# Performance work log

Hardware: AMD Instinct MI355X
Metric: run time of the kernel (lower is better)

## Reference

```python
import jax, jax.numpy as jnp
import numpy as np

# DeepSpeed FixedSparsityConfig defaults (attention='unidirectional')
BLOCK = 16
NUM_LOCAL_BLOCKS = 4   # local window = 4 blocks = 64 tokens
D_MODEL = 1024
N_HEADS = 16
HEAD_DIM = D_MODEL // N_HEADS


def _block_layout(seq_len: int) -> np.ndarray:
    """Token-level boolean mask [S,S] from the fixed unidirectional block layout.
    Allowed iff: (same 4-block local window AND block_k <= block_q) OR
                 (block_k % 4 == 3 AND block_k <= block_q)  (causal global column).
    Same layout for every head (different_layout_per_head=False)."""
    nb = seq_len // BLOCK
    r = np.arange(nb)
    causal = r[None, :] <= r[:, None]
    same_win = (r[:, None] // NUM_LOCAL_BLOCKS) == (r[None, :] // NUM_LOCAL_BLOCKS)
    glob = (r[None, :] % NUM_LOCAL_BLOCKS) == (NUM_LOCAL_BLOCKS - 1)
    layout = (same_win & causal) | (glob & causal)
    return np.kron(layout, np.ones((BLOCK, BLOCK), dtype=bool))


def setup_inputs() -> dict:
    key = jax.random.key(0)
    ks = jax.random.split(key, 7)
    B, S = 2, 2048
    init = 1.0 / np.sqrt(D_MODEL)
    x = jax.random.normal(ks[0], (B, S, D_MODEL), jnp.float32)
    key_padding_mask = jnp.zeros((B, S), jnp.float32)  # additive mask ('add' mode)
    Wq = jax.random.normal(ks[1], (D_MODEL, D_MODEL), jnp.float32) * init
    Wk = jax.random.normal(ks[2], (D_MODEL, D_MODEL), jnp.float32) * init
    Wv = jax.random.normal(ks[3], (D_MODEL, D_MODEL), jnp.float32) * init
    bq = jax.random.normal(ks[4], (D_MODEL,), jnp.float32) * 0.01
    bk = jax.random.normal(ks[5], (D_MODEL,), jnp.float32) * 0.01
    bv = jax.random.normal(ks[6], (D_MODEL,), jnp.float32) * 0.01
    return dict(x=x, key_padding_mask=key_padding_mask,
                Wq=Wq, bq=bq, Wk=Wk, bk=bk, Wv=Wv, bv=bv)


def reference(x, key_padding_mask, Wq, bq, Wk, bk, Wv, bv):
    B, S, D = x.shape
    q = (x @ Wq + bq).reshape(B, S, N_HEADS, HEAD_DIM)
    k = (x @ Wk + bk).reshape(B, S, N_HEADS, HEAD_DIM)
    v = (x @ Wv + bv).reshape(B, S, N_HEADS, HEAD_DIM)
    scale = HEAD_DIM ** -0.5  # DeepSpeed scales by head_size**-0.5 inside softmax
    scores = jnp.einsum('bqhd,bkhd->bhqk', q, k) * scale
    scores = scores + key_padding_mask[:, None, None, :]
    mask = jnp.asarray(_block_layout(S))  # [S,S] bool; absent blocks excluded from softmax
    scores = jnp.where(mask[None, None], scores, -jnp.inf)
    attn = jax.nn.softmax(scores, axis=-1)
    out = jnp.einsum('bhqk,bkhd->bqhd', attn, v)
    return out.reshape(B, S, D)
```

## Files before the change

### kernel.cpp

```cpp
#include <hip/hip_runtime.h>
#include <hip/hip_bf16.h>

typedef __bf16 bf16;
typedef __bf16 bf16x4 __attribute__((ext_vector_type(4)));
typedef __bf16 bf16x8 __attribute__((ext_vector_type(8)));
typedef float  f32x4  __attribute__((ext_vector_type(4)));

#define D_MODEL 1024
#define S_LEN   2048
#define BATCH   2
#define NH      16
#define HD      64
#define NX ((size_t)BATCH * S_LEN * D_MODEL)

__device__ inline void gl_lds16(const bf16* g, bf16* l) {
    __builtin_amdgcn_global_load_lds(
        (const __attribute__((address_space(1))) void*)g,
        (__attribute__((address_space(3))) void*)l, 16, 0, 0);
}

__global__ __launch_bounds__(256) void cvt_x(
    const float* __restrict__ x, bf16* __restrict__ xb)
{
    const size_t base = ((size_t)blockIdx.x * 256 + threadIdx.x) * 8;
    const float4 a = *(const float4*)(x + base);
    const float4 b = *(const float4*)(x + base + 4);
    bf16x8 o;
    o[0] = (bf16)a.x; o[1] = (bf16)a.y; o[2] = (bf16)a.z; o[3] = (bf16)a.w;
    o[4] = (bf16)b.x; o[5] = (bf16)b.y; o[6] = (bf16)b.z; o[7] = (bf16)b.w;
    *(bf16x8*)(xb + base) = o;
}

__global__ __launch_bounds__(256) void wt_cvt(
    const float* __restrict__ Wq, const float* __restrict__ Wk,
    const float* __restrict__ Wv, bf16* __restrict__ Wt)
{
    const int z = blockIdx.z;
    const float* W = (z == 0) ? Wq : (z == 1) ? Wk : Wv;
    const int k0 = blockIdx.y * 64, n0 = blockIdx.x * 64;

    __shared__ bf16 tile[64 * 72];

    const int r16 = threadIdx.x >> 4, c4 = (threadIdx.x & 15) << 2;

#pragma unroll
    for (int rr = 0; rr < 4; ++rr) {
        const int row = rr * 16 + r16;
        const float4 v = *(const float4*)(W + (size_t)(k0 + row) * D_MODEL + n0 + c4);
        bf16x4 o; o[0] = (bf16)v.x; o[1] = (bf16)v.y; o[2] = (bf16)v.z; o[3] = (bf16)v.w;
        *(bf16x4*)(tile + row * 72 + c4) = o;
    }
    __syncthreads();
#pragma unroll
    for (int rr = 0; rr < 4; ++rr) {
        const int row = rr * 16 + r16;
        bf16x4 o;
#pragma unroll
        for (int j = 0; j < 4; ++j) o[j] = tile[(c4 + j) * 72 + row];
        *(bf16x4*)(Wt + (size_t)(z * D_MODEL + n0 + row) * D_MODEL + k0 + c4) = o;
    }
}

__global__ __launch_bounds__(256) void gemm_bt(
    const bf16* __restrict__ Xb, const bf16* __restrict__ Wt,
    const float* __restrict__ bq, const float* __restrict__ bk,
    const float* __restrict__ bv, bf16* __restrict__ QKV)
{
    const int n0 = blockIdx.x * 128, m0 = blockIdx.y * 128;
    const int z  = n0 >> 10;
    const float* bias = (z == 0) ? bq : (z == 1) ? bk : bv;
    const float scale = (z == 0) ? 0.125f : 1.0f;
    bf16* C = QKV + (size_t)z * NX;
    const int ncol0 = n0 & 1023;

    __shared__ bf16 As[128 * 32];
    __shared__ bf16 Bs[128 * 32];

    const int t = threadIdx.x, wave = t >> 6, lane = t & 63;
    const int wm = wave >> 1, wn = wave & 1;
    const int col = lane & 15, quad = lane >> 4;
    const int srow = t >> 2, sc8 = (t & 3) << 3;

    f32x4 acc[4][4] = {};

    for (int k0 = 0; k0 < D_MODEL; k0 += 32) {
        gl_lds16(Xb + (size_t)(m0 + srow) * D_MODEL + k0 + sc8,      As + wave * 512);
        gl_lds16(Xb + (size_t)(m0 + 64 + srow) * D_MODEL + k0 + sc8, As + 2048 + wave * 512);
        gl_lds16(Wt + (size_t)(n0 + srow) * D_MODEL + k0 + sc8,      Bs + wave * 512);
        gl_lds16(Wt + (size_t)(n0 + 64 + srow) * D_MODEL + k0 + sc8, Bs + 2048 + wave * 512);
        __syncthreads();

        bf16x8 a[4], b[4];
#pragma unroll
        for (int mt = 0; mt < 4; ++mt)
            a[mt] = *(const bf16x8*)(As + (wm * 64 + mt * 16 + col) * 32 + quad * 8);
#pragma unroll
        for (int nt = 0; nt < 4; ++nt)
            b[nt] = *(const bf16x8*)(Bs + (wn * 64 + nt * 16 + col) * 32 + quad * 8);
#pragma unroll
        for (int mt = 0; mt < 4; ++mt)
#pragma unroll
            for (int nt = 0; nt < 4; ++nt)
                acc[mt][nt] = __builtin_amdgcn_mfma_f32_16x16x32_bf16(a[mt], b[nt], acc[mt][nt], 0, 0, 0);
        __syncthreads();
    }

#pragma unroll
    for (int nt = 0; nt < 4; ++nt) {
        const int cgw = ncol0 + wn * 64 + nt * 16 + col;
        const float bsv = bias[cgw];
#pragma unroll
        for (int mt = 0; mt < 4; ++mt)
#pragma unroll
            for (int i = 0; i < 4; ++i) {
                const int rg = m0 + wm * 64 + mt * 16 + quad * 4 + i;
                C[(size_t)rg * D_MODEL + cgw] = (bf16)((acc[mt][nt][i] + bsv) * scale);
            }
    }
}

__global__ __launch_bounds__(256) void sparse_attn64(
    const bf16* __restrict__ Q, const bf16* __restrict__ Kv,
    const bf16* __restrict__ Vv, const float* __restrict__ kpm,
    float* __restrict__ out)
{
    const int w = (gridDim.x - 1) - blockIdx.x;
    const int h = blockIdx.y, b = blockIdx.z;
    const int t = threadIdx.x, wavei = t >> 6, lane = t & 63;
    const int col = lane & 15, quad = lane >> 4;
    const int qb = 4 * w + wavei;

    __shared__ bf16 KbS[2][64 * 72];
    __shared__ bf16 VtS[2][64 * 72];
    __shared__ bf16 Ps[4][16 * 72];

    const size_t qrow = ((size_t)(b * S_LEN + qb * 16 + col)) * D_MODEL + h * HD;
    const bf16x8 aq0 = *(const bf16x8*)(Q + qrow + quad * 8);
    const bf16x8 aq1 = *(const bf16x8*)(Q + qrow + 32 + quad * 8);

    f32x4 o[4] = {};
    float lacc[4] = {0.f, 0.f, 0.f, 0.f};

    const int nGlob = (w + 3) >> 2;
    const int niter = nGlob + 1;

    const int srow = t >> 2, sd16 = (t & 3) << 4;
    const int sg = srow >> 4, sr = srow & 15;
    const int p2 = t & 31, dg8 = (t >> 5) << 3;
    const int key0 = 2 * p2, vg = key0 >> 4, vr = key0 & 15;

    auto kb_of = [&](int it, int g) -> int {
        if (it == nGlob) return 4 * w + g;
        const int j = 4 * it + g;
        return (j < w) ? (4 * j + 3) : 3;
    };

    bf16x8 rk0, rk1, rv0, rv1;
    {
        const size_t krow = ((size_t)(b * S_LEN + kb_of(0, sg) * 16 + sr)) * D_MODEL + h * HD + sd16;
        rk0 = *(const bf16x8*)(Kv + krow);
        rk1 = *(const bf16x8*)(Kv + krow + 8);
        const size_t vrow = ((size_t)(b * S_LEN + kb_of(0, vg) * 16 + vr)) * D_MODEL + h * HD + dg8;
        rv0 = *(const bf16x8*)(Vv + vrow);
        rv1 = *(const bf16x8*)(Vv + vrow + D_MODEL);
        *(bf16x8*)(KbS[0] + srow * 72 + sd16)     = rk0;
        *(bf16x8*)(KbS[0] + srow * 72 + sd16 + 8) = rk1;
#pragma unroll
        for (int j = 0; j < 8; ++j) {
            bf16 pr[2] = { rv0[j], rv1[j] };
            *(unsigned int*)(VtS[0] + (dg8 + j) * 72 + key0) = *(unsigned int*)pr;
        }
    }

    for (int it = 0; it < niter; ++it) {
        __syncthreads();
        const int cur = it & 1, nxt = cur ^ 1;
        const bool more = (it + 1 < niter);
        if (more) {
            const size_t krow = ((size_t)(b * S_LEN + kb_of(it + 1, sg) * 16 + sr)) * D_MODEL + h * HD + sd16;
            rk0 = *(const bf16x8*)(Kv + krow);
            rk1 = *(const bf16x8*)(Kv + krow + 8);
            const size_t vrow = ((size_t)(b * S_LEN + kb_of(it + 1, vg) * 16 + vr)) * D_MODEL + h * HD + dg8;
            rv0 = *(const bf16x8*)(Vv + vrow);
            rv1 = *(const bf16x8*)(Vv + vrow + D_MODEL);
        }

        const bf16* Kb = KbS[cur];
        const bf16* Vt = VtS[cur];

        f32x4 s[4];
        float mval[4];
        bool  val[4];
#pragma unroll
        for (int g = 0; g < 4; ++g) {
            int kb;
            if (it == nGlob) { kb = 4 * w + g; val[g] = (g <= wavei); }
            else { const int j = 4 * it + g; val[g] = (j < w); kb = val[g] ? (4 * j + 3) : 3; }
            mval[g] = kpm[b * S_LEN + kb * 16 + col];
            f32x4 z = {};
            const bf16x8 bk0 = *(const bf16x8*)(Kb + (g * 16 + col) * 72 + quad * 8);
            const bf16x8 bk1 = *(const bf16x8*)(Kb + (g * 16 + col) * 72 + 32 + quad * 8);
            z = __builtin_amdgcn_mfma_f32_16x16x32_bf16(aq0, bk0, z, 0, 0, 0);
            s[g] = __builtin_amdgcn_mfma_f32_16x16x32_bf16(aq1, bk1, z, 0, 0, 0);
        }

#pragma unroll
        for (int i = 0; i < 4; ++i) {
#pragma unroll
            for (int g = 0; g < 4; ++g) {
                const float si = val[g] ? (s[g][i] + mval[g]) : -1e30f;
                const float pv = __expf(si);
                lacc[i] += pv;
                Ps[wavei][(quad * 4 + i) * 72 + g * 16 + col] = (bf16)pv;
            }
        }

        const bf16x8 aP0 = *(const bf16x8*)(Ps[wavei] + col * 72 + quad * 8);
        const bf16x8 aP1 = *(const bf16x8*)(Ps[wavei] + col * 72 + 32 + quad * 8);
#pragma unroll
        for (int nt = 0; nt < 4; ++nt) {
            const bf16x8 b0 = *(const bf16x8*)(Vt + (nt * 16 + col) * 72 + quad * 8);
            const bf16x8 b1 = *(const bf16x8*)(Vt + (nt * 16 + col) * 72 + 32 + quad * 8);
            o[nt] = __builtin_amdgcn_mfma_f32_16x16x32_bf16(aP0, b0, o[nt], 0, 0, 0);
            o[nt] = __builtin_amdgcn_mfma_f32_16x16x32_bf16(aP1, b1, o[nt], 0, 0, 0);
        }

        if (more) {
            *(bf16x8*)(KbS[nxt] + srow * 72 + sd16)     = rk0;
            *(bf16x8*)(KbS[nxt] + srow * 72 + sd16 + 8) = rk1;
#pragma unroll
            for (int j = 0; j < 8; ++j) {
                bf16 pr[2] = { rv0[j], rv1[j] };
                *(unsigned int*)(VtS[nxt] + (dg8 + j) * 72 + key0) = *(unsigned int*)pr;
            }
        }
    }

#pragma unroll
    for (int i = 0; i < 4; ++i) {
        float rs = lacc[i];
        rs += __shfl_xor(rs, 1);
        rs += __shfl_xor(rs, 2);
        rs += __shfl_xor(rs, 4);
        rs += __shfl_xor(rs, 8);
        const float inv = 1.0f / rs;
        const int rg = b * S_LEN + qb * 16 + quad * 4 + i;
#pragma unroll
        for (int nt = 0; nt < 4; ++nt)
            out[(size_t)rg * D_MODEL + h * HD + nt * 16 + col] = o[nt][i] * inv;
    }
}

extern "C" void kernel_launch(void* const* d_in, const int* in_sizes, int n_in,
                              void* d_out, int out_size, void* d_ws, size_t ws_size,
                              hipStream_t stream)
{
    const float* x = nullptr; const float* kpm = nullptr;
    const float* Wp[3] = {nullptr, nullptr, nullptr};
    const float* bp[3] = {nullptr, nullptr, nullptr};
    int wn = 0, bn = 0;
    for (int i = 0; i < n_in; ++i) {
        const float* p = (const float*)d_in[i];
        const long s = in_sizes[i];
        if (s == (long)NX)            x = p;
        else if (s == BATCH * S_LEN)  kpm = p;
        else if (s == D_MODEL * D_MODEL && wn < 3) Wp[wn++] = p;
        else if (s == D_MODEL && bn < 3)           bp[bn++] = p;
    }

    bf16* Qb = (bf16*)d_ws;
    bf16* Kb = Qb + NX;
    bf16* Vb = Kb + NX;
    bf16* Xb = (bf16*)d_out;
    bf16* Wt = Xb + NX;
    float* outp = (float*)d_out;

    cvt_x<<<(int)(NX / 8 / 256), 256, 0, stream>>>(x, Xb);
    wt_cvt<<<dim3(16, 16, 3), 256, 0, stream>>>(Wp[0], Wp[1], Wp[2], Wt);

    gemm_bt<<<dim3(3 * D_MODEL / 128, (BATCH * S_LEN) / 128), 256, 0, stream>>>(
        Xb, Wt, bp[0], bp[1], bp[2], Qb);

    sparse_attn64<<<dim3(S_LEN / 64, NH, BATCH), 256, 0, stream>>>(
        Qb, Kb, Vb, kpm, outp);
}
```

Measured before the change: 158.8 us.

## Rewrite QKV GEMM with 4-stage LDS pipeline, swizzle, and 256x192 tiles

Replaces the 128x128 single-buffered QKV projection GEMM with a 256x192 tile, 512-thread kernel using a 4-deep ring of LDS buffers. Global-to-LDS loads are issued three K-steps ahead and gated by explicit vmcnt waits and a single barrier per step. Reads use an XOR chunk swizzle to reduce LDS bank conflicts, and s_setprio is raised around the MFMA block. It aims to hide global load latency and to cut the two barriers per K-step in the old kernel. In exchange it needs 112KB of dynamic shared memory, which limits occupancy, and the grid becomes 256 blocks with uneven fill across the CUs.

```diff
diff --git a/kernel.cpp b/kernel.cpp
--- a/kernel.cpp
+++ b/kernel.cpp
@@ -61,60 +61,108 @@
     }
 }
 
-__global__ __launch_bounds__(256) void gemm_bt(
+#define GNT 32
+
+__device__ __forceinline__ void stage_tile(
+    const bf16* __restrict__ Xb, const bf16* __restrict__ Wt,
+    bf16* __restrict__ sA, bf16* __restrict__ sB,
+    int m0, int n0, int k0, int tid, int wave)
+{
+    {
+        const int ci0 = tid;
+        const int r0 = ci0 >> 2, c0 = (ci0 & 3) ^ ((ci0 >> 3) & 3);
+        gl_lds16(Xb + (size_t)(m0 + r0) * D_MODEL + k0 + c0 * 8, sA + wave * 512);
+        const int ci1 = 512 + tid;
+        const int r1 = ci1 >> 2, c1 = (ci1 & 3) ^ ((ci1 >> 3) & 3);
+        gl_lds16(Xb + (size_t)(m0 + r1) * D_MODEL + k0 + c1 * 8, sA + 4096 + wave * 512);
+    }
+    {
+        const int ci0 = tid;
+        const int r0 = ci0 >> 2, c0 = (ci0 & 3) ^ ((ci0 >> 3) & 3);
+        gl_lds16(Wt + (size_t)(n0 + r0) * D_MODEL + k0 + c0 * 8, sB + wave * 512);
+        if (wave < 4) {
+            const int ci1 = 512 + tid;
+            const int r1 = ci1 >> 2, c1 = (ci1 & 3) ^ ((ci1 >> 3) & 3);
+            gl_lds16(Wt + (size_t)(n0 + r1) * D_MODEL + k0 + c1 * 8, sB + 4096 + wave * 512);
+        }
+    }
+}
+
+template<int VM>
+__device__ __forceinline__ void gemm_tile_body(
+    const bf16* __restrict__ Xb, const bf16* __restrict__ Wt,
+    bf16* __restrict__ As, bf16* __restrict__ Bs,
+    int m0, int n0, int t, int tid, int wave, int wm, int wn,
+    int col, int quad, int pchunk, f32x4 (&acc)[4][6])
+{
+    if constexpr (VM == 8)      asm volatile("s_waitcnt vmcnt(8)" ::: "memory");
+    else if constexpr (VM == 4) asm volatile("s_waitcnt vmcnt(4)" ::: "memory");
+    else                        asm volatile("s_waitcnt vmcnt(0)" ::: "memory");
+    asm volatile("s_barrier" ::: "memory");
+
+    const bf16* bufA = As + (t & 3) * 8192;
+    const bf16* bufB = Bs + (t & 3) * 6144;
+
+    bf16x8 a[4], b[6];
+#pragma unroll
+    for (int mr = 0; mr < 4; ++mr)
+        a[mr] = *(const bf16x8*)(bufA + (wm * 64 + mr * 16 + col) * 32 + pchunk * 8);
+#pragma unroll
+    for (int nr = 0; nr < 6; ++nr)
+        b[nr] = *(const bf16x8*)(bufB + (wn * 96 + nr * 16 + col) * 32 + pchunk * 8);
+
+    if (t + 3 < GNT)
+        stage_tile(Xb, Wt, As + ((t + 3) & 3) * 8192, Bs + ((t + 3) & 3) * 6144,
+                   m0, n0, (t + 3) * 32, tid, wave);
+
+    __builtin_amdgcn_s_setprio(1);
+#pragma unroll
+    for (int mr = 0; mr < 4; ++mr)
+#pragma unroll
+        for (int nr = 0; nr < 6; ++nr)
+            acc[mr][nr] = __builtin_amdgcn_mfma_f32_16x16x32_bf16(a[mr], b[nr], acc[mr][nr], 0, 0, 0);
+    __builtin_amdgcn_s_setprio(0);
+}
+
+__global__ __launch_bounds__(512, 2) void gemm_qkv_dp(
     const bf16* __restrict__ Xb, const bf16* __restrict__ Wt,
     const float* __restrict__ bq, const float* __restrict__ bk,
     const float* __restrict__ bv, bf16* __restrict__ QKV)
 {
-    const int n0 = blockIdx.x * 128, m0 = blockIdx.y * 128;
-    const int z  = n0 >> 10;
-    const float* bias = (z == 0) ? bq : (z == 1) ? bk : bv;
-    const float scale = (z == 0) ? 0.125f : 1.0f;
-    bf16* C = QKV + (size_t)z * NX;
-    const int ncol0 = n0 & 1023;
-
-    __shared__ bf16 As[128 * 32];
-    __shared__ bf16 Bs[128 * 32];
-
-    const int t = threadIdx.x, wave = t >> 6, lane = t & 63;
+    extern __shared__ bf16 smem[];
+    bf16* As = smem;
+    bf16* Bs = smem + 32768;
+
+    const int n0 = blockIdx.x * 192, m0 = blockIdx.y * 256;
+    const int tid = threadIdx.x, wave = tid >> 6, lane = tid & 63;
     const int wm = wave >> 1, wn = wave & 1;
     const int col = lane & 15, quad = lane >> 4;
-    const int srow = t >> 2, sc8 = (t & 3) << 3;
-
-    f32x4 acc[4][4] = {};
-
-    for (int k0 = 0; k0 < D_MODEL; k0 += 32) {
-        gl_lds16(Xb + (size_t)(m0 + srow) * D_MODEL + k0 + sc8,      As + wave * 512);
-        gl_lds16(Xb + (size_t)(m0 + 64 + srow) * D_MODEL + k0 + sc8, As + 2048 + wave * 512);
-        gl_lds16(Wt + (size_t)(n0 + srow) * D_MODEL + k0 + sc8,      Bs + wave * 512);
-        gl_lds16(Wt + (size_t)(n0 + 64 + srow) * D_MODEL + k0 + sc8, Bs + 2048 + wave * 512);
-        __syncthreads();
-
-        bf16x8 a[4], b[4];
-#pragma unroll
-        for (int mt = 0; mt < 4; ++mt)
-            a[mt] = *(const bf16x8*)(As + (wm * 64 + mt * 16 + col) * 32 + quad * 8);
-#pragma unroll
-        for (int nt = 0; nt < 4; ++nt)
-            b[nt] = *(const bf16x8*)(Bs + (wn * 64 + nt * 16 + col) * 32 + quad * 8);
-#pragma unroll
-        for (int mt = 0; mt < 4; ++mt)
-#pragma unroll
-            for (int nt = 0; nt < 4; ++nt)
-                acc[mt][nt] = __builtin_amdgcn_mfma_f32_16x16x32_bf16(a[mt], b[nt], acc[mt][nt], 0, 0, 0);
-        __syncthreads();
-    }
-
-#pragma unroll
-    for (int nt = 0; nt < 4; ++nt) {
-        const int cgw = ncol0 + wn * 64 + nt * 16 + col;
-        const float bsv = bias[cgw];
-#pragma unroll
-        for (int mt = 0; mt < 4; ++mt)
+    const int pchunk = quad ^ ((col >> 1) & 3);
+
+    f32x4 acc[4][6] = {};
+
+    stage_tile(Xb, Wt, As,          Bs,          m0, n0,  0, tid, wave);
+    stage_tile(Xb, Wt, As + 8192,   Bs + 6144,   m0, n0, 32, tid, wave);
+    stage_tile(Xb, Wt, As + 16384,  Bs + 12288,  m0, n0, 64, tid, wave);
+
+    for (int t = 0; t < GNT - 2; ++t)
+        gemm_tile_body<8>(Xb, Wt, As, Bs, m0, n0, t, tid, wave, wm, wn, col, quad, pchunk, acc);
+    gemm_tile_body<4>(Xb, Wt, As, Bs, m0, n0, GNT - 2, tid, wave, wm, wn, col, quad, pchunk, acc);
+    gemm_tile_body<0>(Xb, Wt, As, Bs, m0, n0, GNT - 1, tid, wave, wm, wn, col, quad, pchunk, acc);
+
+#pragma unroll
+    for (int nr = 0; nr < 6; ++nr) {
+        const int cg = n0 + wn * 96 + nr * 16 + col;
+        const int z = cg >> 10, c = cg & 1023;
+        const float bsv = (z == 0 ? bq : (z == 1 ? bk : bv))[c];
+        const float scale = (z == 0) ? 0.125f : 1.0f;
+        bf16* C = QKV + (size_t)z * NX;
+#pragma unroll
+        for (int mr = 0; mr < 4; ++mr)
 #pragma unroll
             for (int i = 0; i < 4; ++i) {
-                const int rg = m0 + wm * 64 + mt * 16 + quad * 4 + i;
-                C[(size_t)rg * D_MODEL + cgw] = (bf16)((acc[mt][nt][i] + bsv) * scale);
+                const int rg = m0 + wm * 64 + mr * 16 + quad * 4 + i;
+                C[(size_t)rg * D_MODEL + c] = (bf16)((acc[mr][nr][i] + bsv) * scale);
             }
     }
 }
@@ -275,10 +323,17 @@
     bf16* Wt = Xb + NX;
     float* outp = (float*)d_out;
 
+    static bool attr_done = false;
+    if (!attr_done) {
+        (void)hipFuncSetAttribute(reinterpret_cast<const void*>(gemm_qkv_dp),
+                                  hipFuncAttributeMaxDynamicSharedMemorySize, 114688);
+        attr_done = true;
+    }
+
     cvt_x<<<(int)(NX / 8 / 256), 256, 0, stream>>>(x, Xb);
     wt_cvt<<<dim3(16, 16, 3), 256, 0, stream>>>(Wp[0], Wp[1], Wp[2], Wt);
 
-    gemm_bt<<<dim3(3 * D_MODEL / 128, (BATCH * S_LEN) / 128), 256, 0, stream>>>(
+    gemm_qkv_dp<<<dim3(16, 16), 512, 114688, stream>>>(
         Xb, Wt, bp[0], bp[1], bp[2], Qb);
 
     sparse_attn64<<<dim3(S_LEN / 64, NH, BATCH), 256, 0, stream>>>(
```

Result: faster. 153.8 us (-3.2%).
